# Kernel tuning notes

Hardware: AMD Instinct MI355X
Metric: run time of the kernel (lower is better)

The kernel has to match this reference:

```python
import jax, jax.numpy as jnp
import numpy as np

DIM = 256
NUM_HEADS = 4
HEAD_DIM = DIM // NUM_HEADS


def setup_inputs() -> dict:
    key = jax.random.key(0)
    ks = jax.random.split(key, 8)
    B, N, C = 4, 2048, DIM
    x = jax.random.normal(ks[0], (B, N, C), dtype=jnp.float32)
    R = jax.random.normal(ks[1], (B, 3, 3), dtype=jnp.float32)
    P = jax.random.normal(ks[2], (N, 3), dtype=jnp.float32)
    s = 1.0 / np.sqrt(C)
    qkv_w = jax.random.normal(ks[3], (3 * C, C), dtype=jnp.float32) * s
    qkv_b = jax.random.normal(ks[4], (3 * C,), dtype=jnp.float32) * 0.02
    proj_w = jax.random.normal(ks[5], (C, C), dtype=jnp.float32) * s
    proj_b = jax.random.normal(ks[6], (C,), dtype=jnp.float32) * 0.02
    pos_scale = jnp.asarray(1.0, dtype=jnp.float32)
    return {"x": x, "R": R, "P": P, "qkv_w": qkv_w, "qkv_b": qkv_b,
            "proj_w": proj_w, "proj_b": proj_b, "pos_scale": pos_scale}


def reference(x, R, P, qkv_w, qkv_b, proj_w, proj_b, pos_scale):
    B, N, C = x.shape
    H, D = NUM_HEADS, HEAD_DIM
    scale = D ** -0.5
    # qkv: (B,N,3C) -> (3,B,H,N,D)
    qkv = (x @ qkv_w.T + qkv_b).reshape(B, N, 3, H, D).transpose(2, 0, 3, 1, 4)
    q, k, v = qkv[0], qkv[1], qkv[2]
    # attention logits (B,H,N,N)
    attn = jnp.einsum('bhid,bhjd->bhij', q, k) * scale
    # positional bias: RP = (R @ P^T)^T -> (B,N,3); bias_ij = dot(RP_i, P_j)
    RP = jnp.einsum('bab,jb->bja', R, P) if False else jnp.einsum('bca,ja->bjc', jnp.swapaxes(R, 1, 2), P)
    RP = jnp.einsum('bcd,jd->bjc', R, P)  # (B,N,3): (R @ P.T).T
    bias = jnp.einsum('bik,jk->bij', RP, P)[:, None, :, :] * pos_scale  # (B,1,N,N) broadcast over heads
    attn = jax.nn.softmax(attn + bias, axis=-1)
    out = jnp.einsum('bhij,bhjd->bhid', attn, v)  # (B,H,N,D)
    out = out.transpose(0, 2, 1, 3).reshape(B, N, C)
    out = out @ proj_w.T + proj_b
    return out
```

## Files before the change

kernel.cpp:

```cpp
#include <hip/hip_runtime.h>
#include <hip/hip_bf16.h>

#define B_ 4
#define N_ 2048
#define C_ 256
#define H_ 4
#define D_ 64

typedef __attribute__((ext_vector_type(8))) short bf16x8;
typedef __attribute__((ext_vector_type(4))) float f32x4;

#define LOG2E 1.4426950408889634f

static __device__ inline unsigned short f2bf(float f) {
    unsigned u = __builtin_bit_cast(unsigned, f);
    unsigned r = (u + 0x7fffu + ((u >> 16) & 1u)) >> 16;
    return (unsigned short)r;
}
static __device__ inline float bf2f(unsigned short h) {
    unsigned u = ((unsigned)h) << 16;
    return __builtin_bit_cast(float, u);
}
static __device__ inline unsigned pack2(float a, float b) {
    __hip_bfloat162 h = __float22bfloat162_rn(make_float2(a, b));
    unsigned u;
    __builtin_memcpy(&u, &h, 4);
    return u;
}
static __device__ inline bf16x8 ld_frag(const unsigned short* p) {
    return __builtin_bit_cast(bf16x8, *(const uint4*)p);
}

__global__ __launch_bounds__(256) void cvt_kernel(
    const float* __restrict__ x, const float* __restrict__ qkv_w,
    const float* __restrict__ proj_w,
    unsigned short* __restrict__ xb, unsigned short* __restrict__ wqb,
    unsigned short* __restrict__ wpb)
{
    const int bid = blockIdx.x, tid = threadIdx.x;
    const float* s; unsigned short* d; int i;
    if (bid < 1024)      { s = x;      d = xb;  i = (bid * 256 + tid) * 8; }
    else if (bid < 1120) { s = qkv_w;  d = wqb; i = ((bid - 1024) * 256 + tid) * 8; }
    else                 { s = proj_w; d = wpb; i = ((bid - 1120) * 256 + tid) * 8; }
    float4 a = *(const float4*)(s + i);
    float4 b = *(const float4*)(s + i + 4);
    uint4 u;
    u.x = pack2(a.x, a.y); u.y = pack2(a.z, a.w);
    u.z = pack2(b.x, b.y); u.w = pack2(b.z, b.w);
    *(uint4*)(d + i) = u;
}

__global__ __launch_bounds__(256) void qkv_gemm(
    const unsigned short* __restrict__ xb, const unsigned short* __restrict__ wb,
    const float* __restrict__ bias, unsigned short* __restrict__ qb,
    unsigned short* __restrict__ kb, unsigned short* __restrict__ vt)
{
    __shared__ __align__(16) unsigned short As[128 * 40];
    __shared__ __align__(16) unsigned short Bs[128 * 40];
    const int m0 = blockIdx.x * 128, o0 = blockIdx.y * 128;
    const int tid = threadIdx.x;
    const int wave = tid >> 6, lane = tid & 63, quad = lane >> 4, l16 = lane & 15;
    const int wy = wave >> 1, wx = wave & 1;

    f32x4 acc[4][4];
    #pragma unroll
    for (int i = 0; i < 4; ++i)
        #pragma unroll
        for (int j = 0; j < 4; ++j) acc[i][j] = (f32x4){0.f, 0.f, 0.f, 0.f};

    const int srow = tid >> 1, soff = (tid & 1) * 16;

    for (int k0 = 0; k0 < 256; k0 += 32) {
        __syncthreads();
        {
            const unsigned short* sa = &xb[(size_t)(m0 + srow) * 256 + k0 + soff];
            const unsigned short* sb = &wb[(size_t)(o0 + srow) * 256 + k0 + soff];
            *(uint4*)&As[srow * 40 + soff + 0] = *(const uint4*)(sa + 0);
            *(uint4*)&As[srow * 40 + soff + 8] = *(const uint4*)(sa + 8);
            *(uint4*)&Bs[srow * 40 + soff + 0] = *(const uint4*)(sb + 0);
            *(uint4*)&Bs[srow * 40 + soff + 8] = *(const uint4*)(sb + 8);
        }
        __syncthreads();
        bf16x8 a[4], b[4];
        #pragma unroll
        for (int mt = 0; mt < 4; ++mt) a[mt] = ld_frag(&As[(wy * 64 + mt * 16 + l16) * 40 + quad * 8]);
        #pragma unroll
        for (int nt = 0; nt < 4; ++nt) b[nt] = ld_frag(&Bs[(wx * 64 + nt * 16 + l16) * 40 + quad * 8]);
        #pragma unroll
        for (int mt = 0; mt < 4; ++mt)
            #pragma unroll
            for (int nt = 0; nt < 4; ++nt)
                acc[mt][nt] = __builtin_amdgcn_mfma_f32_16x16x32_bf16(a[mt], b[nt], acc[mt][nt], 0, 0, 0);
    }

    const int sec = o0 + wx * 64;
    const int three = sec >> 8;
    const int h = (sec >> 6) & 3;
    const int b = m0 >> 11;
    float bv[4];
    #pragma unroll
    for (int nt = 0; nt < 4; ++nt) bv[nt] = bias[sec + nt * 16 + l16];

    if (three == 2) {
        const int n64 = (m0 + wy * 64) & 2047;
        const size_t bh64 = ((size_t)b * H_ + h) * 64;
        #pragma unroll
        for (int nt = 0; nt < 4; ++nt) {
            int d = nt * 16 + l16;
            #pragma unroll
            for (int r = 0; r < 4; ++r) {
                ushort4 v;
                v.x = f2bf(acc[0][nt][r] + bv[nt]);
                v.y = f2bf(acc[1][nt][r] + bv[nt]);
                v.z = f2bf(acc[2][nt][r] + bv[nt]);
                v.w = f2bf(acc[3][nt][r] + bv[nt]);
                *(ushort4*)&vt[(bh64 + d) * N_ + n64 + 16 * quad + 4 * r] = v;
            }
        }
    } else {
        unsigned short* dst = (three == 0) ? qb : kb;
        float sc = (three == 0) ? (0.125f * LOG2E) : 1.0f;
        #pragma unroll
        for (int mt = 0; mt < 4; ++mt)
            #pragma unroll
            for (int r = 0; r < 4; ++r) {
                int n = (m0 + wy * 64 + mt * 16 + quad * 4 + r) & 2047;
                size_t rowbase = (((size_t)b * H_ + h) * N_ + n) * D_;
                #pragma unroll
                for (int nt = 0; nt < 4; ++nt)
                    dst[rowbase + nt * 16 + l16] = f2bf((acc[mt][nt][r] + bv[nt]) * sc);
            }
    }
}

#define LDK 72
#define LDKX 104

__global__ __launch_bounds__(256) void attn_kernel(
    const unsigned short* __restrict__ qb, const unsigned short* __restrict__ kb,
    const unsigned short* __restrict__ vt,
    const float* __restrict__ Rm, const float* __restrict__ Pm,
    const float* __restrict__ ps_ptr,
    unsigned short* __restrict__ Opart, float* __restrict__ ml)
{
    __shared__ __align__(16) unsigned short Ks[64 * LDKX];
    __shared__ __align__(16) unsigned short Vs[64 * LDK];
    __shared__ __align__(16) unsigned short Ps[64 * LDK];

    const int bh = blockIdx.y;
    const int b = bh >> 2;
    const int i0 = blockIdx.x * 64;
    const int split = blockIdx.z;
    const int tid = threadIdx.x;
    const int wave = tid >> 6, lane = tid & 63;
    const int quad = lane >> 4, l16 = lane & 15;
    const float ps = ps_ptr[0];

    const size_t base = (size_t)bh * N_ * D_;
    const unsigned short* qg = qb + base;
    const unsigned short* kg = kb + base;
    const unsigned short* vg = vt + base;

    if (tid < 64) {
        uint4 z = {0u, 0u, 0u, 0u};
        *(uint4*)&Ks[tid * LDKX + 80] = z;
        *(uint4*)&Ks[tid * LDKX + 88] = z;
    }

    const int qrow = i0 + wave * 16 + l16;
    bf16x8 aq[3];
    #pragma unroll
    for (int ks = 0; ks < 2; ++ks)
        aq[ks] = ld_frag(&qg[(size_t)qrow * D_ + ks * 32 + quad * 8]);

    {
        float p0 = Pm[qrow * 3 + 0], p1 = Pm[qrow * 3 + 1], p2 = Pm[qrow * 3 + 2];
        float sc = ps * LOG2E;
        unsigned short ah[3], al[3];
        #pragma unroll
        for (int c = 0; c < 3; ++c) {
            float a = (Rm[b * 9 + c * 3 + 0] * p0 + Rm[b * 9 + c * 3 + 1] * p1
                     + Rm[b * 9 + c * 3 + 2] * p2) * sc;
            ah[c] = f2bf(a);
            al[c] = f2bf(a - bf2f(ah[c]));
        }
        bf16x8 e = (bf16x8){0,0,0,0,0,0,0,0};
        if (quad == 0) {
            e[0] = (short)ah[0]; e[1] = (short)ah[1]; e[2] = (short)ah[2];
            e[3] = (short)ah[0]; e[4] = (short)ah[1]; e[5] = (short)ah[2];
            e[6] = (short)al[0]; e[7] = (short)al[1];
        } else if (quad == 1) {
            e[0] = (short)al[2];
        }
        aq[2] = e;
    }

    const bf16x8 ones = (bf16x8){0x3F80,0x3F80,0x3F80,0x3F80,0x3F80,0x3F80,0x3F80,0x3F80};

    float m_run = -1e30f;
    f32x4 o_acc[4], lacc;
    #pragma unroll
    for (int t = 0; t < 4; ++t) o_acc[t] = (f32x4){0.f, 0.f, 0.f, 0.f};
    lacc = (f32x4){0.f, 0.f, 0.f, 0.f};

    const int jbeg = split * (N_ / 2);
    const int NT = (N_ / 2) / 64;

    for (int jt = 0; jt < NT; ++jt) {
        const int j0 = jbeg + jt * 64;
        __syncthreads();
        #pragma unroll
        for (int rr = 0; rr < 2; ++rr) {
            int c = tid + rr * 256;
            int row = c >> 3, off = (c & 7) * 8;
            *(uint4*)&Ks[row * LDKX + off] = *(const uint4*)&kg[(size_t)(j0 + row) * D_ + off];
            *(uint4*)&Vs[row * LDK + off] = *(const uint4*)&vg[(size_t)row * N_ + j0 + off];
        }
        if (tid < 64) {
            const float* pp = &Pm[(size_t)(j0 + tid) * 3];
            float p0 = pp[0], p1 = pp[1], p2 = pp[2];
            unsigned u0 = f2bf(p0), u1 = f2bf(p1), u2 = f2bf(p2);
            unsigned v0 = f2bf(p0 - bf2f((unsigned short)u0));
            unsigned v1 = f2bf(p1 - bf2f((unsigned short)u1));
            unsigned v2 = f2bf(p2 - bf2f((unsigned short)u2));
            uint4 lo, hi;
            lo.x = u0 | (u1 << 16); lo.y = u2 | (v0 << 16);
            lo.z = v1 | (v2 << 16); lo.w = u0 | (u1 << 16);
            hi.x = u2; hi.y = 0u; hi.z = 0u; hi.w = 0u;
            *(uint4*)&Ks[tid * LDKX + 64] = lo;
            *(uint4*)&Ks[tid * LDKX + 72] = hi;
        }
        __syncthreads();

        f32x4 s[4];
        #pragma unroll
        for (int t = 0; t < 4; ++t) {
            f32x4 c = {0.f, 0.f, 0.f, 0.f};
            #pragma unroll
            for (int ks = 0; ks < 3; ++ks) {
                bf16x8 bk = ld_frag(&Ks[(l16 + 16 * t) * LDKX + ks * 32 + quad * 8]);
                c = __builtin_amdgcn_mfma_f32_16x16x32_bf16(aq[ks], bk, c, 0, 0, 0);
            }
            s[t] = c;
        }

        float mx = m_run;
        #pragma unroll
        for (int t = 0; t < 4; ++t)
            #pragma unroll
            for (int r = 0; r < 4; ++r)
                mx = fmaxf(mx, s[t][r]);
        #pragma unroll
        for (int off = 1; off < 64; off <<= 1)
            mx = fmaxf(mx, __shfl_xor(mx, off));
        const float alpha = exp2f(m_run - mx);
        m_run = mx;

        #pragma unroll
        for (int r = 0; r < 4; ++r) {
            float p0 = exp2f(s[0][r] - mx), p1 = exp2f(s[1][r] - mx);
            float p2 = exp2f(s[2][r] - mx), p3 = exp2f(s[3][r] - mx);
            uint2 w;
            w.x = pack2(p0, p1);
            w.y = pack2(p2, p3);
            *(uint2*)&Ps[(wave * 16 + quad * 4 + r) * LDK + 4 * l16] = w;
        }

        if (alpha < 1.0f) {
            #pragma unroll
            for (int t = 0; t < 4; ++t)
                #pragma unroll
                for (int r = 0; r < 4; ++r)
                    o_acc[t][r] *= alpha;
            #pragma unroll
            for (int r = 0; r < 4; ++r) lacc[r] *= alpha;
        }

        #pragma unroll
        for (int ks = 0; ks < 2; ++ks) {
            bf16x8 ap = ld_frag(&Ps[(wave * 16 + l16) * LDK + ks * 32 + quad * 8]);
            #pragma unroll
            for (int t = 0; t < 4; ++t) {
                bf16x8 bv = ld_frag(&Vs[(l16 + 16 * t) * LDK + ks * 32 + quad * 8]);
                o_acc[t] = __builtin_amdgcn_mfma_f32_16x16x32_bf16(ap, bv, o_acc[t], 0, 0, 0);
            }
            lacc = __builtin_amdgcn_mfma_f32_16x16x32_bf16(ap, ones, lacc, 0, 0, 0);
        }
    }

    const size_t pbase = (size_t)(split * 16 + bh) * N_;
    #pragma unroll
    for (int r = 0; r < 4; ++r) {
        int row = i0 + wave * 16 + quad * 4 + r;
        #pragma unroll
        for (int t = 0; t < 4; ++t)
            Opart[(pbase + row) * D_ + l16 + 16 * t] = f2bf(o_acc[t][r]);
        if (l16 == 0) {
            float2* mlp = (float2*)ml;
            mlp[pbase + row] = make_float2(m_run, lacc[r]);
        }
    }
}

__global__ __launch_bounds__(256) void proj_gemm(
    const unsigned short* __restrict__ Opart, const float* __restrict__ ml,
    const unsigned short* __restrict__ wb, const float* __restrict__ bias,
    float* __restrict__ out)
{
    __shared__ __align__(16) unsigned short As[64 * 40];
    __shared__ __align__(16) unsigned short Bs[64 * 40];
    const int m0 = blockIdx.x * 64, o0 = blockIdx.y * 64;
    const int tid = threadIdx.x;
    const int wave = tid >> 6, lane = tid & 63, quad = lane >> 4, l16 = lane & 15;
    const float2* mlp = (const float2*)ml;

    const int srow = tid >> 2, scb = (tid & 3) * 8;
    const int sm = m0 + srow, sb = sm >> 11, sn = sm & 2047;

    float w1h[4], w2h[4];
    #pragma unroll
    for (int h = 0; h < 4; ++h) {
        size_t r1 = (size_t)(sb * 4 + h) * N_ + sn;
        float2 ml1 = mlp[r1], ml2 = mlp[r1 + 16 * N_];
        float mm = fmaxf(ml1.x, ml2.x);
        float w1 = exp2f(ml1.x - mm), w2 = exp2f(ml2.x - mm);
        float inv = 1.f / (ml1.y * w1 + ml2.y * w2);
        w1h[h] = w1 * inv; w2h[h] = w2 * inv;
    }

    f32x4 acc[4];
    #pragma unroll
    for (int j = 0; j < 4; ++j) acc[j] = (f32x4){0.f, 0.f, 0.f, 0.f};

    for (int k0 = 0; k0 < 256; k0 += 32) {
        const int h = k0 >> 6;
        const int d0 = (k0 & 63) + scb;
        __syncthreads();
        {
            size_t r1 = (size_t)(sb * 4 + h) * N_ + sn;
            union { uint4 u; unsigned short s[8]; } a1, a2;
            a1.u = *(const uint4*)&Opart[r1 * D_ + d0];
            a2.u = *(const uint4*)&Opart[(r1 + 16 * N_) * D_ + d0];
            float w1 = w1h[h], w2 = w2h[h];
            uint4 mv;
            unsigned* mp = (unsigned*)&mv;
            #pragma unroll
            for (int j = 0; j < 4; ++j)
                mp[j] = pack2(bf2f(a1.s[2*j]) * w1 + bf2f(a2.s[2*j]) * w2,
                              bf2f(a1.s[2*j+1]) * w1 + bf2f(a2.s[2*j+1]) * w2);
            *(uint4*)&As[srow * 40 + scb] = mv;
            *(uint4*)&Bs[srow * 40 + scb] = *(const uint4*)&wb[(size_t)(o0 + srow) * 256 + k0 + scb];
        }
        __syncthreads();
        bf16x8 a = ld_frag(&As[(wave * 16 + l16) * 40 + quad * 8]);
        #pragma unroll
        for (int nt = 0; nt < 4; ++nt) {
            bf16x8 b = ld_frag(&Bs[(nt * 16 + l16) * 40 + quad * 8]);
            acc[nt] = __builtin_amdgcn_mfma_f32_16x16x32_bf16(a, b, acc[nt], 0, 0, 0);
        }
    }

    float bv[4];
    #pragma unroll
    for (int nt = 0; nt < 4; ++nt) bv[nt] = bias[o0 + nt * 16 + l16];
    #pragma unroll
    for (int r = 0; r < 4; ++r) {
        int m = m0 + wave * 16 + quad * 4 + r;
        #pragma unroll
        for (int nt = 0; nt < 4; ++nt)
            out[(size_t)m * 256 + o0 + nt * 16 + l16] = acc[nt][r] + bv[nt];
    }
}

extern "C" void kernel_launch(void* const* d_in, const int* in_sizes, int n_in,
                              void* d_out, int out_size, void* d_ws, size_t ws_size,
                              hipStream_t stream) {
    const float* x       = (const float*)d_in[0];
    const float* Rm      = (const float*)d_in[1];
    const float* Pm      = (const float*)d_in[2];
    const float* qkv_w   = (const float*)d_in[3];
    const float* qkv_b   = (const float*)d_in[4];
    const float* proj_w  = (const float*)d_in[5];
    const float* proj_b  = (const float*)d_in[6];
    const float* pos_scl = (const float*)d_in[7];
    float* out = (float*)d_out;

    const size_t NE = (size_t)B_ * H_ * N_ * D_;
    unsigned short* xb    = (unsigned short*)d_ws;
    unsigned short* wqb   = xb   + NE;
    unsigned short* wpb   = wqb  + 768 * 256;
    unsigned short* qb    = wpb  + 256 * 256;
    unsigned short* kb    = qb   + NE;
    unsigned short* vtb   = kb   + NE;
    unsigned short* opart = vtb  + NE;
    float*          mlb   = (float*)(opart + 2 * NE);

    cvt_kernel<<<1152, 256, 0, stream>>>(x, qkv_w, proj_w, xb, wqb, wpb);
    qkv_gemm<<<dim3(64, 6), 256, 0, stream>>>(xb, wqb, qkv_b, qb, kb, vtb);
    attn_kernel<<<dim3(32, 16, 2), 256, 0, stream>>>(qb, kb, vtb, Rm, Pm, pos_scl, opart, mlb);
    proj_gemm<<<dim3(128, 4), 256, 0, stream>>>(opart, mlb, wpb, proj_b, out);
}
```

Baseline: 140.2 us.

## Prefetch K/V tiles into registers, XOR-swizzle LDS, lazy softmax rescale

Result: slower. 155.0 us (+10.6%).

```diff
diff --git a/kernel.cpp b/kernel.cpp
--- a/kernel.cpp
+++ b/kernel.cpp
@@ -133,8 +133,8 @@
     }
 }
 
-#define LDK 72
-#define LDKX 104
+#define LDH 128
+#define LDV 64
 
 __global__ __launch_bounds__(256) void attn_kernel(
     const unsigned short* __restrict__ qb, const unsigned short* __restrict__ kb,
@@ -143,9 +143,9 @@
     const float* __restrict__ ps_ptr,
     unsigned short* __restrict__ Opart, float* __restrict__ ml)
 {
-    __shared__ __align__(16) unsigned short Ks[64 * LDKX];
-    __shared__ __align__(16) unsigned short Vs[64 * LDK];
-    __shared__ __align__(16) unsigned short Ps[64 * LDK];
+    __shared__ __align__(16) unsigned short Ks[64 * LDH];
+    __shared__ __align__(16) unsigned short Vs[64 * LDV];
+    __shared__ __align__(16) unsigned short Ps[64 * LDV];
 
     const int bh = blockIdx.y;
     const int b = bh >> 2;
@@ -154,6 +154,7 @@
     const int tid = threadIdx.x;
     const int wave = tid >> 6, lane = tid & 63;
     const int quad = lane >> 4, l16 = lane & 15;
+    const int x7 = l16 & 7;
     const float ps = ps_ptr[0];
 
     const size_t base = (size_t)bh * N_ * D_;
@@ -161,10 +162,11 @@
     const unsigned short* kg = kb + base;
     const unsigned short* vg = vt + base;
 
-    if (tid < 64) {
-        uint4 z = {0u, 0u, 0u, 0u};
-        *(uint4*)&Ks[tid * LDKX + 80] = z;
-        *(uint4*)&Ks[tid * LDKX + 88] = z;
+    {
+        const uint4 z = {0u, 0u, 0u, 0u};
+        int u0 = tid, u1 = tid + 256;
+        *(uint4*)&Ks[(u0 >> 3) * LDH + 64 + (u0 & 7) * 8] = z;
+        *(uint4*)&Ks[(u1 >> 3) * LDH + 64 + (u1 & 7) * 8] = z;
     }
 
     const int qrow = i0 + wave * 16 + l16;
@@ -206,45 +208,75 @@
     const int jbeg = split * (N_ / 2);
     const int NT = (N_ / 2) / 64;
 
-    for (int jt = 0; jt < NT; ++jt) {
-        const int j0 = jbeg + jt * 64;
-        __syncthreads();
-        #pragma unroll
-        for (int rr = 0; rr < 2; ++rr) {
-            int c = tid + rr * 256;
-            int row = c >> 3, off = (c & 7) * 8;
-            *(uint4*)&Ks[row * LDKX + off] = *(const uint4*)&kg[(size_t)(j0 + row) * D_ + off];
-            *(uint4*)&Vs[row * LDK + off] = *(const uint4*)&vg[(size_t)row * N_ + j0 + off];
-        }
+    const int r0 = tid >> 3, r1 = r0 + 32;
+    const int sl = tid & 7;
+    const int so = sl * 8;
+    const int kw0 = r0 * LDH + ((sl ^ (r0 & 7)) * 8);
+    const int kw1 = r1 * LDH + ((sl ^ (r1 & 7)) * 8);
+    const int vw0 = r0 * LDV + ((sl ^ (r0 & 7)) * 8);
+    const int vw1 = r1 * LDV + ((sl ^ (r1 & 7)) * 8);
+
+    const unsigned short* kp0 = kg + (size_t)(jbeg + r0) * D_ + so;
+    const unsigned short* kp1 = kg + (size_t)(jbeg + r1) * D_ + so;
+    const unsigned short* vp0 = vg + (size_t)r0 * N_ + jbeg + so;
+    const unsigned short* vp1 = vg + (size_t)r1 * N_ + jbeg + so;
+    const float* pp = Pm + (size_t)(jbeg + tid) * 3;
+
+    uint4 rk0, rk1, rv0, rv1;
+    uint4 elo, ehi;
+
+    auto LOAD = [&]() {
+        rk0 = *(const uint4*)kp0; rk1 = *(const uint4*)kp1;
+        rv0 = *(const uint4*)vp0; rv1 = *(const uint4*)vp1;
         if (tid < 64) {
-            const float* pp = &Pm[(size_t)(j0 + tid) * 3];
             float p0 = pp[0], p1 = pp[1], p2 = pp[2];
             unsigned u0 = f2bf(p0), u1 = f2bf(p1), u2 = f2bf(p2);
             unsigned v0 = f2bf(p0 - bf2f((unsigned short)u0));
             unsigned v1 = f2bf(p1 - bf2f((unsigned short)u1));
             unsigned v2 = f2bf(p2 - bf2f((unsigned short)u2));
-            uint4 lo, hi;
-            lo.x = u0 | (u1 << 16); lo.y = u2 | (v0 << 16);
-            lo.z = v1 | (v2 << 16); lo.w = u0 | (u1 << 16);
-            hi.x = u2; hi.y = 0u; hi.z = 0u; hi.w = 0u;
-            *(uint4*)&Ks[tid * LDKX + 64] = lo;
-            *(uint4*)&Ks[tid * LDKX + 72] = hi;
-        }
-        __syncthreads();
+            elo.x = u0 | (u1 << 16); elo.y = u2 | (v0 << 16);
+            elo.z = v1 | (v2 << 16); elo.w = u0 | (u1 << 16);
+            ehi.x = u2; ehi.y = 0u; ehi.z = 0u; ehi.w = 0u;
+        }
+    };
+
+    LOAD();
+
+    for (int jt = 0; jt < NT; ++jt) {
+        __syncthreads();
+        *(uint4*)&Ks[kw0] = rk0;
+        *(uint4*)&Ks[kw1] = rk1;
+        *(uint4*)&Vs[vw0] = rv0;
+        *(uint4*)&Vs[vw1] = rv1;
+        if (tid < 64) {
+            *(uint4*)&Ks[tid * LDH + ((8 ^ (tid & 7)) * 8)] = elo;
+            *(uint4*)&Ks[tid * LDH + ((9 ^ (tid & 7)) * 8)] = ehi;
+        }
+        __syncthreads();
+
+        if (jt + 1 < NT) {
+            kp0 += 64 * D_; kp1 += 64 * D_;
+            vp0 += 64;      vp1 += 64;
+            pp  += 64 * 3;
+            LOAD();
+        }
 
         f32x4 s[4];
+        __builtin_amdgcn_s_setprio(1);
         #pragma unroll
         for (int t = 0; t < 4; ++t) {
             f32x4 c = {0.f, 0.f, 0.f, 0.f};
+            const int rb = (l16 + 16 * t) * LDH;
             #pragma unroll
             for (int ks = 0; ks < 3; ++ks) {
-                bf16x8 bk = ld_frag(&Ks[(l16 + 16 * t) * LDKX + ks * 32 + quad * 8]);
+                bf16x8 bk = ld_frag(&Ks[rb + (((ks * 4 + quad) ^ x7) * 8)]);
                 c = __builtin_amdgcn_mfma_f32_16x16x32_bf16(aq[ks], bk, c, 0, 0, 0);
             }
             s[t] = c;
         }
-
-        float mx = m_run;
+        __builtin_amdgcn_s_setprio(0);
+
+        float mx = s[0][0];
         #pragma unroll
         for (int t = 0; t < 4; ++t)
             #pragma unroll
@@ -253,20 +285,9 @@
         #pragma unroll
         for (int off = 1; off < 64; off <<= 1)
             mx = fmaxf(mx, __shfl_xor(mx, off));
-        const float alpha = exp2f(m_run - mx);
-        m_run = mx;
-
-        #pragma unroll
-        for (int r = 0; r < 4; ++r) {
-            float p0 = exp2f(s[0][r] - mx), p1 = exp2f(s[1][r] - mx);
-            float p2 = exp2f(s[2][r] - mx), p3 = exp2f(s[3][r] - mx);
-            uint2 w;
-            w.x = pack2(p0, p1);
-            w.y = pack2(p2, p3);
-            *(uint2*)&Ps[(wave * 16 + quad * 4 + r) * LDK + 4 * l16] = w;
-        }
-
-        if (alpha < 1.0f) {
+
+        if (mx > m_run + 8.0f) {
+            const float alpha = exp2f(m_run - mx);
             #pragma unroll
             for (int t = 0; t < 4; ++t)
                 #pragma unroll
@@ -274,18 +295,35 @@
                     o_acc[t][r] *= alpha;
             #pragma unroll
             for (int r = 0; r < 4; ++r) lacc[r] *= alpha;
-        }
-
+            m_run = mx;
+        }
+
+        #pragma unroll
+        for (int r = 0; r < 4; ++r) {
+            float p0 = exp2f(s[0][r] - m_run), p1 = exp2f(s[1][r] - m_run);
+            float p2 = exp2f(s[2][r] - m_run), p3 = exp2f(s[3][r] - m_run);
+            uint2 w;
+            w.x = pack2(p0, p1);
+            w.y = pack2(p2, p3);
+            const int prow = quad * 4 + r;
+            *(uint2*)&Ps[(wave * 16 + prow) * LDV
+                         + (((l16 >> 1) ^ (prow & 7)) * 8) + (l16 & 1) * 4] = w;
+        }
+
+        __builtin_amdgcn_s_setprio(1);
         #pragma unroll
         for (int ks = 0; ks < 2; ++ks) {
-            bf16x8 ap = ld_frag(&Ps[(wave * 16 + l16) * LDK + ks * 32 + quad * 8]);
+            bf16x8 ap = ld_frag(&Ps[(wave * 16 + l16) * LDV
+                                    + (((ks * 4 + quad) ^ x7) * 8)]);
             #pragma unroll
             for (int t = 0; t < 4; ++t) {
-                bf16x8 bv = ld_frag(&Vs[(l16 + 16 * t) * LDK + ks * 32 + quad * 8]);
+                bf16x8 bv = ld_frag(&Vs[(l16 + 16 * t) * LDV
+                                        + (((ks * 4 + quad) ^ x7) * 8)]);
                 o_acc[t] = __builtin_amdgcn_mfma_f32_16x16x32_bf16(ap, bv, o_acc[t], 0, 0, 0);
             }
             lacc = __builtin_amdgcn_mfma_f32_16x16x32_bf16(ap, ones, lacc, 0, 0, 0);
         }
+        __builtin_amdgcn_s_setprio(0);
     }
 
     const size_t pbase = (size_t)(split * 16 + bh) * N_;
```

## Double-buffer attention K/V tiles via async global-to-LDS loads with XOR swizzle

Applied to the files above, without the earlier changes.

After: 145.2 us. 1.04x slower.

```diff
diff --git a/kernel.cpp b/kernel.cpp
--- a/kernel.cpp
+++ b/kernel.cpp
@@ -30,14 +30,36 @@
 static __device__ inline bf16x8 ld_frag(const unsigned short* p) {
     return __builtin_bit_cast(bf16x8, *(const uint4*)p);
 }
+static __device__ inline void gload_lds16(const unsigned short* g, unsigned short* l) {
+    __builtin_amdgcn_global_load_lds(
+        (const __attribute__((address_space(1))) unsigned int*)(g),
+        (__attribute__((address_space(3))) unsigned int*)(l),
+        16, 0, 0);
+}
 
 __global__ __launch_bounds__(256) void cvt_kernel(
     const float* __restrict__ x, const float* __restrict__ qkv_w,
-    const float* __restrict__ proj_w,
+    const float* __restrict__ proj_w, const float* __restrict__ Pm,
     unsigned short* __restrict__ xb, unsigned short* __restrict__ wqb,
-    unsigned short* __restrict__ wpb)
+    unsigned short* __restrict__ wpb, unsigned short* __restrict__ eb)
 {
     const int bid = blockIdx.x, tid = threadIdx.x;
+    if (bid >= 1152) {
+        const int n = (bid - 1152) * 256 + tid;
+        const float* pp = Pm + n * 3;
+        float p0 = pp[0], p1 = pp[1], p2 = pp[2];
+        unsigned u0 = f2bf(p0), u1 = f2bf(p1), u2 = f2bf(p2);
+        unsigned v0 = f2bf(p0 - bf2f((unsigned short)u0));
+        unsigned v1 = f2bf(p1 - bf2f((unsigned short)u1));
+        unsigned v2 = f2bf(p2 - bf2f((unsigned short)u2));
+        uint4 lo, hi;
+        lo.x = u0 | (u1 << 16); lo.y = u2 | (v0 << 16);
+        lo.z = v1 | (v2 << 16); lo.w = u0 | (u1 << 16);
+        hi.x = u2; hi.y = 0u; hi.z = 0u; hi.w = 0u;
+        *(uint4*)&eb[n * 16 + 0] = lo;
+        *(uint4*)&eb[n * 16 + 8] = hi;
+        return;
+    }
     const float* s; unsigned short* d; int i;
     if (bid < 1024)      { s = x;      d = xb;  i = (bid * 256 + tid) * 8; }
     else if (bid < 1120) { s = qkv_w;  d = wqb; i = ((bid - 1024) * 256 + tid) * 8; }
@@ -133,18 +155,17 @@
     }
 }
 
-#define LDK 72
-#define LDKX 104
+#define LDK 64
 
 __global__ __launch_bounds__(256) void attn_kernel(
     const unsigned short* __restrict__ qb, const unsigned short* __restrict__ kb,
-    const unsigned short* __restrict__ vt,
+    const unsigned short* __restrict__ vt, const unsigned short* __restrict__ eb,
     const float* __restrict__ Rm, const float* __restrict__ Pm,
     const float* __restrict__ ps_ptr,
     unsigned short* __restrict__ Opart, float* __restrict__ ml)
 {
-    __shared__ __align__(16) unsigned short Ks[64 * LDKX];
-    __shared__ __align__(16) unsigned short Vs[64 * LDK];
+    __shared__ __align__(16) unsigned short Ks[2][64 * LDK];
+    __shared__ __align__(16) unsigned short Vs[2][64 * LDK];
     __shared__ __align__(16) unsigned short Ps[64 * LDK];
 
     const int bh = blockIdx.y;
@@ -154,6 +175,7 @@
     const int tid = threadIdx.x;
     const int wave = tid >> 6, lane = tid & 63;
     const int quad = lane >> 4, l16 = lane & 15;
+    const int x7 = l16 & 7;
     const float ps = ps_ptr[0];
 
     const size_t base = (size_t)bh * N_ * D_;
@@ -161,11 +183,30 @@
     const unsigned short* kg = kb + base;
     const unsigned short* vg = vt + base;
 
-    if (tid < 64) {
-        uint4 z = {0u, 0u, 0u, 0u};
-        *(uint4*)&Ks[tid * LDKX + 80] = z;
-        *(uint4*)&Ks[tid * LDKX + 88] = z;
-    }
+    const int jbeg = split * (N_ / 2);
+    const int NT = (N_ / 2) / 64;
+
+    const int rl = lane >> 3, sl = lane & 7;
+    const int swz = (sl ^ rl) * 8;
+    const unsigned short* kq = kg + (size_t)(jbeg + wave * 16 + rl) * D_ + swz;
+    const unsigned short* vq = vg + (size_t)(wave * 16 + rl) * N_ + jbeg + swz;
+    const unsigned short* ep = eb + (size_t)(jbeg + l16) * 16 + (quad & 1) * 8;
+
+    auto ISSUE = [&](int nb) {
+        unsigned short* kd = &Ks[nb][(wave * 16) * LDK];
+        unsigned short* vd = &Vs[nb][(wave * 16) * LDK];
+        gload_lds16(kq,           kd);
+        gload_lds16(kq + 8 * D_,  kd + 8 * LDK);
+        gload_lds16(vq,           vd);
+        gload_lds16(vq + 8 * N_,  vd + 8 * LDK);
+    };
+
+    ISSUE(0);
+    kq += 64 * D_; vq += 64;
+    bf16x8 ereg[4];
+    #pragma unroll
+    for (int t = 0; t < 4; ++t) ereg[t] = ld_frag(ep + t * 256);
+    ep += 64 * 16;
 
     const int qrow = i0 + wave * 16 + l16;
     bf16x8 aq[3];
@@ -203,70 +244,50 @@
     for (int t = 0; t < 4; ++t) o_acc[t] = (f32x4){0.f, 0.f, 0.f, 0.f};
     lacc = (f32x4){0.f, 0.f, 0.f, 0.f};
 
-    const int jbeg = split * (N_ / 2);
-    const int NT = (N_ / 2) / 64;
-
     for (int jt = 0; jt < NT; ++jt) {
-        const int j0 = jbeg + jt * 64;
+        const int cur = jt & 1;
+        asm volatile("s_waitcnt vmcnt(0)" ::: "memory");
         __syncthreads();
-        #pragma unroll
-        for (int rr = 0; rr < 2; ++rr) {
-            int c = tid + rr * 256;
-            int row = c >> 3, off = (c & 7) * 8;
-            *(uint4*)&Ks[row * LDKX + off] = *(const uint4*)&kg[(size_t)(j0 + row) * D_ + off];
-            *(uint4*)&Vs[row * LDK + off] = *(const uint4*)&vg[(size_t)row * N_ + j0 + off];
-        }
-        if (tid < 64) {
-            const float* pp = &Pm[(size_t)(j0 + tid) * 3];
-            float p0 = pp[0], p1 = pp[1], p2 = pp[2];
-            unsigned u0 = f2bf(p0), u1 = f2bf(p1), u2 = f2bf(p2);
-            unsigned v0 = f2bf(p0 - bf2f((unsigned short)u0));
-            unsigned v1 = f2bf(p1 - bf2f((unsigned short)u1));
-            unsigned v2 = f2bf(p2 - bf2f((unsigned short)u2));
-            uint4 lo, hi;
-            lo.x = u0 | (u1 << 16); lo.y = u2 | (v0 << 16);
-            lo.z = v1 | (v2 << 16); lo.w = u0 | (u1 << 16);
-            hi.x = u2; hi.y = 0u; hi.z = 0u; hi.w = 0u;
-            *(uint4*)&Ks[tid * LDKX + 64] = lo;
-            *(uint4*)&Ks[tid * LDKX + 72] = hi;
-        }
-        __syncthreads();
+        if (jt + 1 < NT) {
+            ISSUE(cur ^ 1);
+            kq += 64 * D_; vq += 64;
+        }
 
         f32x4 s[4];
+        __builtin_amdgcn_s_setprio(1);
         #pragma unroll
         for (int t = 0; t < 4; ++t) {
+            const int rb = (l16 + 16 * t) * LDK;
             f32x4 c = {0.f, 0.f, 0.f, 0.f};
             #pragma unroll
-            for (int ks = 0; ks < 3; ++ks) {
-                bf16x8 bk = ld_frag(&Ks[(l16 + 16 * t) * LDKX + ks * 32 + quad * 8]);
+            for (int ks = 0; ks < 2; ++ks) {
+                bf16x8 bk = ld_frag(&Ks[cur][rb + (((ks * 4 + quad) ^ x7) * 8)]);
                 c = __builtin_amdgcn_mfma_f32_16x16x32_bf16(aq[ks], bk, c, 0, 0, 0);
             }
+            c = __builtin_amdgcn_mfma_f32_16x16x32_bf16(aq[2], ereg[t], c, 0, 0, 0);
             s[t] = c;
         }
-
-        float mx = m_run;
+        __builtin_amdgcn_s_setprio(0);
+
+        if (jt + 1 < NT) {
+            #pragma unroll
+            for (int t = 0; t < 4; ++t) ereg[t] = ld_frag(ep + t * 256);
+            ep += 64 * 16;
+        }
+
+        float mx = s[0][0];
         #pragma unroll
         for (int t = 0; t < 4; ++t)
             #pragma unroll
             for (int r = 0; r < 4; ++r)
                 mx = fmaxf(mx, s[t][r]);
         #pragma unroll
-        for (int off = 1; off < 64; off <<= 1)
+        for (int off = 1; off < 16; off <<= 1)
             mx = fmaxf(mx, __shfl_xor(mx, off));
-        const float alpha = exp2f(m_run - mx);
-        m_run = mx;
-
-        #pragma unroll
-        for (int r = 0; r < 4; ++r) {
-            float p0 = exp2f(s[0][r] - mx), p1 = exp2f(s[1][r] - mx);
-            float p2 = exp2f(s[2][r] - mx), p3 = exp2f(s[3][r] - mx);
-            uint2 w;
-            w.x = pack2(p0, p1);
-            w.y = pack2(p2, p3);
-            *(uint2*)&Ps[(wave * 16 + quad * 4 + r) * LDK + 4 * l16] = w;
-        }
-
-        if (alpha < 1.0f) {
+
+        if (__any(mx > m_run + 8.0f)) {
+            float mnew = fmaxf(m_run, mx);
+            float alpha = exp2f(m_run - mnew);
             #pragma unroll
             for (int t = 0; t < 4; ++t)
                 #pragma unroll
@@ -274,18 +295,35 @@
                     o_acc[t][r] *= alpha;
             #pragma unroll
             for (int r = 0; r < 4; ++r) lacc[r] *= alpha;
-        }
-
+            m_run = mnew;
+        }
+
+        #pragma unroll
+        for (int r = 0; r < 4; ++r) {
+            float p0 = exp2f(s[0][r] - m_run), p1 = exp2f(s[1][r] - m_run);
+            float p2 = exp2f(s[2][r] - m_run), p3 = exp2f(s[3][r] - m_run);
+            uint2 w;
+            w.x = pack2(p0, p1);
+            w.y = pack2(p2, p3);
+            const int prow = quad * 4 + r;
+            *(uint2*)&Ps[(wave * 16 + prow) * LDK
+                         + (((l16 >> 1) ^ (prow & 7)) * 8) + (l16 & 1) * 4] = w;
+        }
+
+        __builtin_amdgcn_s_setprio(1);
         #pragma unroll
         for (int ks = 0; ks < 2; ++ks) {
-            bf16x8 ap = ld_frag(&Ps[(wave * 16 + l16) * LDK + ks * 32 + quad * 8]);
+            bf16x8 ap = ld_frag(&Ps[(wave * 16 + l16) * LDK
+                                    + (((ks * 4 + quad) ^ x7) * 8)]);
             #pragma unroll
             for (int t = 0; t < 4; ++t) {
-                bf16x8 bv = ld_frag(&Vs[(l16 + 16 * t) * LDK + ks * 32 + quad * 8]);
+                bf16x8 bv = ld_frag(&Vs[cur][(l16 + 16 * t) * LDK
+                                             + (((ks * 4 + quad) ^ x7) * 8)]);
                 o_acc[t] = __builtin_amdgcn_mfma_f32_16x16x32_bf16(ap, bv, o_acc[t], 0, 0, 0);
             }
             lacc = __builtin_amdgcn_mfma_f32_16x16x32_bf16(ap, ones, lacc, 0, 0, 0);
         }
+        __builtin_amdgcn_s_setprio(0);
     }
 
     const size_t pbase = (size_t)(split * 16 + bh) * N_;
@@ -394,9 +432,10 @@
     unsigned short* vtb   = kb   + NE;
     unsigned short* opart = vtb  + NE;
     float*          mlb   = (float*)(opart + 2 * NE);
-
-    cvt_kernel<<<1152, 256, 0, stream>>>(x, qkv_w, proj_w, xb, wqb, wpb);
+    unsigned short* eb    = (unsigned short*)(mlb + 2 * 16 * N_ * 2);
+
+    cvt_kernel<<<1160, 256, 0, stream>>>(x, qkv_w, proj_w, Pm, xb, wqb, wpb, eb);
     qkv_gemm<<<dim3(64, 6), 256, 0, stream>>>(xb, wqb, qkv_b, qb, kb, vtb);
-    attn_kernel<<<dim3(32, 16, 2), 256, 0, stream>>>(qb, kb, vtb, Rm, Pm, pos_scl, opart, mlb);
+    attn_kernel<<<dim3(32, 16, 2), 256, 0, stream>>>(qb, kb, vtb, eb, Rm, Pm, pos_scl, opart, mlb);
     proj_gemm<<<dim3(128, 4), 256, 0, stream>>>(opart, mlb, wpb, proj_b, out);
 }
```
